# Kernel tuning notes

Hardware: AMD Instinct MI355X
Metric: run time of the kernel (lower is better)

The kernel has to match this reference:

```python
import jax, jax.numpy as jnp
import numpy as np

B, S, D, H, F = 8, 1024, 1024, 16, 4096
DH = D // H
EPS = 1e-8
NEG_INF = -1e30


def setup_inputs() -> dict:
    key = jax.random.key(0)
    ks = jax.random.split(key, 12)
    x = jax.random.normal(ks[0], (B, S, D), jnp.float32)
    # variable valid lengths in [S//2, S]; True = keep (valid token)
    lengths = jax.random.randint(ks[1], (B,), S // 2, S + 1)
    src_key_padding_mask = jnp.arange(S)[None, :] < lengths[:, None]
    rel_pos_bias = 0.02 * jax.random.normal(ks[2], (1, H, S, S), jnp.float32)
    w = lambda k, sh, std: std * jax.random.normal(k, sh, jnp.float32)
    std = D ** -0.5
    return {
        'x': x,
        'src_key_padding_mask': src_key_padding_mask,
        'rel_pos_bias': rel_pos_bias,
        'Wq': w(ks[3], (D, D), std),
        'Wk': w(ks[4], (D, D), std),
        'Wv': w(ks[5], (D, D), std),
        'Wo': w(ks[6], (D, D), std),
        'g1': jnp.ones((D,), jnp.float32),
        'g2': jnp.ones((D,), jnp.float32),
        'W1': w(ks[7], (D, F), std),
        'b1': jnp.zeros((F,), jnp.float32),
        'W2': w(ks[8], (F, F and D), F ** -0.5),
        'b2': jnp.zeros((D,), jnp.float32),
    }


def rmsnorm(x, g):
    # x / sqrt(mean(x^2) + eps) * g   (no mean subtraction)
    ms = jnp.mean(x * x, axis=-1, keepdims=True)
    return x * jax.lax.rsqrt(ms + EPS) * g


def attention(h, kpm, rel_pos_bias, Wq, Wk, Wv, Wo):
    b, s, d = h.shape
    q = (h @ Wq).reshape(b, s, H, DH)
    k = (h @ Wk).reshape(b, s, H, DH)
    v = (h @ Wv).reshape(b, s, H, DH)
    scores = jnp.einsum('bqhd,bkhd->bhqk', q, k) / np.sqrt(DH)
    scores = scores + rel_pos_bias
    scores = jnp.where(kpm[:, None, None, :], scores, NEG_INF)
    attn = jax.nn.softmax(scores, axis=-1)
    out = jnp.einsum('bhqk,bkhd->bqhd', attn, v).reshape(b, s, d)
    return out @ Wo


def reference(x, src_key_padding_mask, rel_pos_bias,
              Wq, Wk, Wv, Wo, g1, g2, W1, b1, W2, b2):
    h = rmsnorm(x, g1)
    x = x + attention(h, src_key_padding_mask, rel_pos_bias, Wq, Wk, Wv, Wo)
    h = rmsnorm(x, g2)
    ff = jax.nn.relu(h @ W1 + b1) @ W2 + b2
    return x + ff
```

## Files before the change

### kernel.cpp

```cpp
#include <hip/hip_runtime.h>
#include <stdint.h>

typedef __bf16 bf16;
typedef __bf16 bf16x4 __attribute__((ext_vector_type(4)));
typedef __bf16 bf16x8 __attribute__((ext_vector_type(8)));
typedef float f32x4 __attribute__((ext_vector_type(4)));

constexpr int Bz = 8, S = 1024, D = 1024, NH = 16, DH = 64, F = 4096;

__device__ __forceinline__ bool is_f32(const uint16_t* dt) { return dt[0] == 0; }

__device__ __forceinline__ void ld4(const void* p, size_t idx, bool f32, float o[4]) {
  if (f32) {
    float4 v = *(const float4*)((const float*)p + idx);
    o[0] = v.x; o[1] = v.y; o[2] = v.z; o[3] = v.w;
  } else {
    bf16x4 v = *(const bf16x4*)((const bf16*)p + idx);
    o[0] = v[0]; o[1] = v[1]; o[2] = v[2]; o[3] = v[3];
  }
}

__device__ __forceinline__ float ld1(const void* p, size_t idx, bool f32) {
  return f32 ? ((const float*)p)[idx] : (float)((const bf16*)p)[idx];
}

__device__ __forceinline__ void gload_lds16(const bf16* g, bf16* l) {
  __builtin_amdgcn_global_load_lds(
      (const __attribute__((address_space(1))) void*)g,
      (__attribute__((address_space(3))) void*)l, 16, 0, 0);
}

__global__ void prep_all(const void* __restrict__ sq, const void* __restrict__ sk,
                         const void* __restrict__ sv, const void* __restrict__ so,
                         const void* __restrict__ s1, const void* __restrict__ s2,
                         bf16* __restrict__ dq, bf16* __restrict__ dk,
                         bf16* __restrict__ dv, bf16* __restrict__ do_,
                         bf16* __restrict__ d1, bf16* __restrict__ d2,
                         const unsigned char* __restrict__ mask,
                         int* __restrict__ lengths,
                         const void* __restrict__ rpb, bf16* __restrict__ biasb,
                         const uint16_t* __restrict__ dt) {
  __shared__ bf16 tile[64][65];
  __shared__ int sred[4];
  bool f32 = is_f32(dt);
  int t = blockIdx.x;
  int tx = threadIdx.x, ty = threadIdx.y;
  if (t >= 3080) {
    size_t i = ((size_t)(t - 3080) * 256 + ty * 16 + tx) * 4;
    float v[4];
    ld4(rpb, i, f32, v);
    bf16x4 o;
#pragma unroll
    for (int j = 0; j < 4; j++) o[j] = (bf16)(v[j] * 1.4426950408889634f);
    *(bf16x4*)(biasb + i) = o;
    return;
  }
  if (t >= 3072) {
    int b = t - 3072;
    int tid = ty * 16 + tx;
    int esz = (mask[1] == 1) ? 1 : ((mask[1] != 0) ? 2 : 4);
    int cnt = 0;
    for (int s = tid; s < S; s += 256) {
      const unsigned char* p = mask + ((size_t)b * S + s) * esz;
      unsigned v = 0;
      for (int j = 0; j < esz; j++) v |= p[j];
      cnt += (v != 0) ? 1 : 0;
    }
#pragma unroll
    for (int m = 32; m >= 1; m >>= 1) cnt += __shfl_xor(cnt, m);
    if ((tid & 63) == 0) sred[tid >> 6] = cnt;
    __syncthreads();
    if (tid == 0) lengths[b] = sred[0] + sred[1] + sred[2] + sred[3];
    return;
  }
  const void* src;
  bf16* dst;
  int R, C, gx, base;
  if (t < 1024) {
    int wsel = t >> 8;
    base = wsel << 8;
    src = wsel == 0 ? sq : wsel == 1 ? sk : wsel == 2 ? sv : so;
    dst = wsel == 0 ? dq : wsel == 1 ? dk : wsel == 2 ? dv : do_;
    R = 1024; C = 1024; gx = 16;
  } else if (t < 2048) {
    base = 1024; src = s1; dst = d1; R = 1024; C = 4096; gx = 64;
  } else {
    base = 2048; src = s2; dst = d2; R = 4096; C = 1024; gx = 16;
  }
  int rel = t - base;
  int c0 = (rel % gx) * 64, r0 = (rel / gx) * 64;
#pragma unroll
  for (int i = 0; i < 4; i++) {
    int r = ty * 4 + i;
    float v[4];
    ld4(src, (size_t)(r0 + r) * C + c0 + tx * 4, f32, v);
#pragma unroll
    for (int j = 0; j < 4; j++) tile[r][tx * 4 + j] = (bf16)v[j];
  }
  __syncthreads();
#pragma unroll
  for (int i = 0; i < 4; i++) {
    int rr = ty * 4 + i;
    bf16x4 ov;
#pragma unroll
    for (int j = 0; j < 4; j++) ov[j] = tile[tx * 4 + j][rr];
    *(bf16x4*)(dst + (size_t)(c0 + rr) * R + r0 + tx * 4) = ov;
  }
}

template <bool ADD>
__global__ void rmsnorm_kernel(const void* __restrict__ xv, const bf16* __restrict__ add,
                               const void* __restrict__ gv, bf16* __restrict__ y,
                               const uint16_t* __restrict__ dt) {
  bool f32 = is_f32(dt);
  int row = blockIdx.x, t = threadIdx.x;
  float xf[4];
  ld4(xv, (size_t)row * D + t * 4, f32, xf);
  if (ADD) {
    bf16x4 a = *(const bf16x4*)(add + (size_t)row * D + t * 4);
#pragma unroll
    for (int j = 0; j < 4; j++) xf[j] += (float)a[j];
  }
  float ss = xf[0] * xf[0] + xf[1] * xf[1] + xf[2] * xf[2] + xf[3] * xf[3];
#pragma unroll
  for (int m = 32; m >= 1; m >>= 1) ss += __shfl_xor(ss, m);
  __shared__ float sred[4];
  if ((t & 63) == 0) sred[t >> 6] = ss;
  __syncthreads();
  float tot = sred[0] + sred[1] + sred[2] + sred[3];
  float scale = rsqrtf(tot * (1.0f / D) + 1e-8f);
  float gf[4];
  ld4(gv, (size_t)t * 4, f32, gf);
  bf16x4 ov;
#pragma unroll
  for (int j = 0; j < 4; j++) ov[j] = (bf16)(xf[j] * scale * gf[j]);
  *(bf16x4*)(y + (size_t)row * D + t * 4) = ov;
}

template <bool BIAS, bool RELU, bool RES1, bool RES2, bool OUTEXT, bool VT>
__global__ void gemm_nt(const bf16* __restrict__ A, const bf16* __restrict__ Bt,
                        void* __restrict__ Cv, const void* __restrict__ biasv,
                        const void* __restrict__ res1, const bf16* __restrict__ res2,
                        int M, int N, int K, const uint16_t* __restrict__ dt) {
  bool f32 = is_f32(dt);
  __shared__ bf16 As[2 * 4096];
  __shared__ bf16 Bs[2 * 4096];
  const int tid = threadIdx.x, lane = tid & 63, w = tid >> 6;
  const int wm = w >> 1, wn = w & 1;
  const int lid = blockIdx.x;
  const int bm = ((lid & 7) << 3) + ((lid >> 3) & 7);
  const int bn = lid >> 6;
  const int quad = lane >> 4, c = lane & 15;

  f32x4 acc[4][4];
#pragma unroll
  for (int i = 0; i < 4; i++)
#pragma unroll
    for (int j = 0; j < 4; j++)
#pragma unroll
      for (int r = 0; r < 4; r++) acc[i][j][r] = 0.f;

  const bf16* gA = A + (size_t)(bm * 128 + w * 16 + (lane >> 2)) * K + (lane & 3) * 8;
  const bf16* gB = Bt + (size_t)(bn * 128 + w * 16 + (lane >> 2)) * K + (lane & 3) * 8;
  bf16* lA = As + w * 512;
  bf16* lB = Bs + w * 512;
  const size_t rstep = (size_t)64 * K;

  int aoff[4], boff[4];
#pragma unroll
  for (int i = 0; i < 4; i++) {
    aoff[i] = (wm * 64 + i * 16 + c) * 32 + quad * 8;
    boff[i] = (wn * 64 + i * 16 + c) * 32 + quad * 8;
  }

  for (int k0 = 0; k0 < K; k0 += 64) {
    __syncthreads();
#pragma unroll
    for (int p = 0; p < 2; p++) {
      gload_lds16(gA + p * 32, lA + p * 4096);
      gload_lds16(gA + p * 32 + rstep, lA + p * 4096 + 2048);
      gload_lds16(gB + p * 32, lB + p * 4096);
      gload_lds16(gB + p * 32 + rstep, lB + p * 4096 + 2048);
    }
    gA += 64;
    gB += 64;
    __syncthreads();
#pragma unroll
    for (int p = 0; p < 2; p++) {
      bf16x8 af[4], bfr[4];
#pragma unroll
      for (int i = 0; i < 4; i++) af[i] = *(const bf16x8*)(As + p * 4096 + aoff[i]);
#pragma unroll
      for (int i = 0; i < 4; i++) bfr[i] = *(const bf16x8*)(Bs + p * 4096 + boff[i]);
#pragma unroll
      for (int i = 0; i < 4; i++)
#pragma unroll
        for (int j = 0; j < 4; j++)
          acc[i][j] = __builtin_amdgcn_mfma_f32_16x16x32_bf16(af[i], bfr[j], acc[i][j], 0, 0, 0);
    }
  }

  const int m0 = bm * 128 + wm * 64, n0 = bn * 128 + wn * 64;
#pragma unroll
  for (int i = 0; i < 4; i++) {
#pragma unroll
    for (int j = 0; j < 4; j++) {
      int col = n0 + j * 16 + c;
      if (VT) {
        int row0 = m0 + i * 16 + quad * 4;
        int bb = row0 >> 10, s0 = row0 & 1023;
        int hh = col >> 6, dd = col & 63;
        bf16x4 ov;
#pragma unroll
        for (int r = 0; r < 4; r++) ov[r] = (bf16)acc[i][j][r];
        *(bf16x4*)((bf16*)Cv + ((size_t)((bb << 4) + hh) * 64 + dd) * 1024 + s0) = ov;
      } else {
        float bv = BIAS ? ld1(biasv, col, f32) : 0.f;
#pragma unroll
        for (int r = 0; r < 4; r++) {
          int row = m0 + i * 16 + quad * 4 + r;
          size_t idx = (size_t)row * N + col;
          float vv = acc[i][j][r] + bv;
          if (RELU) vv = fmaxf(vv, 0.f);
          if (RES1) vv += ld1(res1, idx, f32);
          if (RES2) vv += (float)res2[idx];
          if (OUTEXT && f32) ((float*)Cv)[idx] = vv;
          else ((bf16*)Cv)[idx] = (bf16)vv;
        }
      }
    }
  }
}

#define SYNC()                            \
  do {                                    \
    __builtin_amdgcn_sched_barrier(0);    \
    __builtin_amdgcn_s_barrier();         \
    __builtin_amdgcn_sched_barrier(0);    \
  } while (0)
#define VMW(n)                                              \
  do {                                                      \
    asm volatile("s_waitcnt vmcnt(" #n ")" ::: "memory");   \
    __builtin_amdgcn_sched_barrier(0);                      \
  } while (0)

#define STA_(nb, rowbase, kb)                                                  \
  do {                                                                         \
    gload_lds16(Ag + (size_t)(rowbase) * K + (kb), &Abuf[nb][(rowbase) * 64]); \
    gload_lds16(Ag + (size_t)((rowbase) + 8) * K + (kb),                       \
                &Abuf[nb][((rowbase) + 8) * 64]);                              \
  } while (0)
#define STB_(nb, rowbase, kb)                                                  \
  do {                                                                         \
    gload_lds16(Bg + (size_t)(rowbase) * K + (kb), &Bbuf[nb][(rowbase) * 64]); \
    gload_lds16(Bg + (size_t)((rowbase) + 8) * K + (kb),                       \
                &Bbuf[nb][((rowbase) + 8) * 64]);                              \
  } while (0)
#define RDA_(MQ, fr, bufsel)                                                          \
  do {                                                                                \
    _Pragma("unroll") for (int ii = 0; ii < 4; ii++) {                                \
      int arow = wm * 128 + ((MQ)*4 + ii) * 16 + c;                                   \
      fr[ii][0] = *(const bf16x8*)&Abuf[bufsel][arow * 64 + ((quad ^ sx) * 8)];       \
      fr[ii][1] = *(const bf16x8*)&Abuf[bufsel][arow * 64 + (((4 + quad) ^ sx) * 8)]; \
    }                                                                                 \
  } while (0)
#define RDB_(NQ, fr, bufsel)                                                          \
  do {                                                                                \
    _Pragma("unroll") for (int jj = 0; jj < 2; jj++) {                                \
      int brow = wn * 64 + ((NQ)*2 + jj) * 16 + c;                                    \
      fr[jj][0] = *(const bf16x8*)&Bbuf[bufsel][brow * 64 + ((quad ^ sx) * 8)];       \
      fr[jj][1] = *(const bf16x8*)&Bbuf[bufsel][brow * 64 + (((4 + quad) ^ sx) * 8)]; \
    }                                                                                 \
  } while (0)

template <int MQ, int NQ>
__device__ __forceinline__ void mm_phase(f32x4 (&acc)[8][4], const bf16x8 (&afr)[4][2],
                                         const bf16x8 (&bfr)[2][2]) {
#pragma unroll
  for (int ii = 0; ii < 4; ii++)
#pragma unroll
    for (int jj = 0; jj < 2; jj++) {
      acc[MQ * 4 + ii][NQ * 2 + jj] = __builtin_amdgcn_mfma_f32_16x16x32_bf16(
          afr[ii][0], bfr[jj][0], acc[MQ * 4 + ii][NQ * 2 + jj], 0, 0, 0);
      acc[MQ * 4 + ii][NQ * 2 + jj] = __builtin_amdgcn_mfma_f32_16x16x32_bf16(
          afr[ii][1], bfr[jj][1], acc[MQ * 4 + ii][NQ * 2 + jj], 0, 0, 0);
    }
}

template <bool BIAS, bool RELU, bool QKV>
__global__ void __launch_bounds__(512, 2) gemm256(
    const bf16* __restrict__ A, const bf16* __restrict__ Bt, bf16* __restrict__ C,
    bf16* __restrict__ C2, const void* __restrict__ biasv, int N, int K,
    const uint16_t* __restrict__ dt) {
  bool f32 = is_f32(dt);
  __shared__ bf16 Abuf[2][256 * 64];
  __shared__ bf16 Bbuf[2][256 * 64];
  const int tid = threadIdx.x, lane = tid & 63, w = tid >> 6;
  const int wm = w >> 2, wn = w & 3;
  const int quad = lane >> 4, c = lane & 15;
  const int sx = c & 7;
  const int nbn = N >> 8;
  const int nwg = gridDim.x;
  const int sid = (blockIdx.x & 7) * (nwg >> 3) + (blockIdx.x >> 3);
  const int bm = sid / nbn, bn = sid % nbn;

  const int lrow = lane >> 3;
  const int lslot = ((lane & 7) ^ lrow) * 8;
  const bf16* Ag = A + (size_t)(bm * 256 + lrow) * K + lslot;
  const bf16* Bg = Bt + (size_t)(bn * 256 + lrow) * K + lslot;

  const int ra0 = wm * 128 + wn * 16;
  const int ra1 = ra0 + 64;
  const int rb0 = (wn >> 1) * 128 + (wn & 1) * 64 + wm * 16;
  const int rb1 = rb0 + 32;

  f32x4 acc[8][4];
#pragma unroll
  for (int i = 0; i < 8; i++)
#pragma unroll
    for (int j = 0; j < 4; j++)
#pragma unroll
      for (int r = 0; r < 4; r++) acc[i][j][r] = 0.f;

  const int nt = K >> 6;

  STA_(0, ra0, 0);
  STA_(0, ra1, 0);
  STB_(0, rb0, 0);
  STB_(0, rb1, 0);
  STA_(1, ra0, 64);
  VMW(2);
  SYNC();

  for (int t = 0; t < nt; ++t) {
    const int buf = t & 1, nb = buf ^ 1;
    const int kb1 = (t + 1) << 6, kb2 = (t + 2) << 6;
    const bool st1 = (t + 1 < nt), st2 = (t + 2 < nt);
    bf16x8 afr[4][2], bfr0[2][2], bfr1[2][2];
    RDA_(0, afr, buf);
    RDB_(0, bfr0, buf);
    if (st1) STA_(nb, ra1, kb1);
    SYNC();
    __builtin_amdgcn_s_setprio(1);
    mm_phase<0, 0>(acc, afr, bfr0);
    __builtin_amdgcn_s_setprio(0);
    VMW(2);
    SYNC();
    RDB_(1, bfr1, buf);
    if (st1) STB_(nb, rb0, kb1);
    SYNC();
    __builtin_amdgcn_s_setprio(1);
    mm_phase<0, 1>(acc, afr, bfr1);
    __builtin_amdgcn_s_setprio(0);
    SYNC();
    RDA_(1, afr, buf);
    if (st2) STA_(buf, ra0, kb2);
    SYNC();
    __builtin_amdgcn_s_setprio(1);
    mm_phase<1, 0>(acc, afr, bfr0);
    __builtin_amdgcn_s_setprio(0);
    SYNC();
    if (st1) STB_(nb, rb1, kb1);
    SYNC();
    __builtin_amdgcn_s_setprio(1);
    mm_phase<1, 1>(acc, afr, bfr1);
    __builtin_amdgcn_s_setprio(0);
    VMW(4);
    SYNC();
  }

  const int m0 = bm * 256 + wm * 128, n0 = bn * 256 + wn * 64;
  if (QKV && n0 >= 2048) {
#pragma unroll
    for (int fi = 0; fi < 8; fi++)
#pragma unroll
      for (int fj = 0; fj < 4; fj++) {
        int vcol = n0 + fj * 16 + c - 2048;
        int hh = vcol >> 6, dd = vcol & 63;
        int row0 = m0 + fi * 16 + quad * 4;
        int bb = row0 >> 10, s0 = row0 & 1023;
        bf16x4 ov;
#pragma unroll
        for (int r = 0; r < 4; r++) ov[r] = (bf16)acc[fi][fj][r];
        *(bf16x4*)(C2 + ((size_t)((bb << 4) + hh) * 64 + dd) * 1024 + s0) = ov;
      }
    return;
  }
  const int ldc = QKV ? 2048 : N;
#pragma unroll
  for (int fi = 0; fi < 8; fi++)
#pragma unroll
    for (int fj = 0; fj < 4; fj++) {
      int col = n0 + fj * 16 + c;
      float bv = BIAS ? ld1(biasv, col, f32) : 0.f;
#pragma unroll
      for (int r = 0; r < 4; r++) {
        int row = m0 + fi * 16 + quad * 4 + r;
        float vv = acc[fi][fj][r] + bv;
        if (RELU) vv = fmaxf(vv, 0.f);
        C[(size_t)row * ldc + col] = (bf16)vv;
      }
    }
}

__global__ void __launch_bounds__(256) attn_kernel(
    const bf16* __restrict__ qk, const bf16* __restrict__ vt,
    const bf16* __restrict__ bias, const int* __restrict__ lengths,
    bf16* __restrict__ out) {
  __shared__ bf16 QPs[64 * 72];
  __shared__ bf16 Ks[2][64][72];
  __shared__ bf16 Vs[2][64][72];
  const int tid = threadIdx.x, lane = tid & 63, w = tid >> 6;
  const int id = blockIdx.x;
  const int qt = id >> 7, b = (id >> 4) & 7, h = id & 15;
  const int len = lengths[b];
  const int quad = lane >> 4, c = lane & 15;
  const int r4 = tid >> 2, c4 = tid & 3;

  {
    size_t qrow = (size_t)(b * S + qt * 64 + r4) * 2048 + h * 64 + c4 * 8;
    *(bf16x8*)&QPs[r4 * 72 + c4 * 8] = *(const bf16x8*)&qk[qrow];
    *(bf16x8*)&QPs[r4 * 72 + 32 + c4 * 8] = *(const bf16x8*)&qk[qrow + 32];
  }
  __syncthreads();
  const bf16x8 a0 = *(const bf16x8*)&QPs[(w * 16 + c) * 72 + quad * 8];
  const bf16x8 a1 = *(const bf16x8*)&QPs[(w * 16 + c) * 72 + 32 + quad * 8];

  bf16* Pw = QPs + w * 16 * 72;
  const int xsw = (quad & 2) << 3;
  const int xsr = (c & 8) << 1;

  float l_[4] = {0.f, 0.f, 0.f, 0.f};
  f32x4 o[4];
#pragma unroll
  for (int ni = 0; ni < 4; ni++)
#pragma unroll
    for (int r = 0; r < 4; r++) o[ni][r] = 0.f;

  const bf16* bbp = bias + (size_t)h * S * S + (size_t)(qt * 64 + w * 16 + quad * 4) * S;
  const int nkt = (len + 63) >> 6;

  const size_t KSTEP = (size_t)64 * 2048;
  const bf16* gk = qk + (size_t)(b * S + r4) * 2048 + 1024 + h * 64 + c4 * 8;
  const bf16* gv = vt + ((size_t)((b * 16 + h) * 64 + r4)) * 1024 + c4 * 8;
  bf16x8 kr0 = *(const bf16x8*)gk;
  bf16x8 kr1 = *(const bf16x8*)(gk + 32);
  bf16x8 vr0 = *(const bf16x8*)gv;
  bf16x8 vr1 = *(const bf16x8*)(gv + 32);
  gk += KSTEP;
  gv += 64;
  *(bf16x8*)&Ks[0][r4][c4 * 8] = kr0;
  *(bf16x8*)&Ks[0][r4][32 + c4 * 8] = kr1;
  *(bf16x8*)&Vs[0][r4][c4 * 8] = vr0;
  *(bf16x8*)&Vs[0][r4][32 + c4 * 8] = vr1;
  if (nkt > 1) {
    kr0 = *(const bf16x8*)gk;
    kr1 = *(const bf16x8*)(gk + 32);
    vr0 = *(const bf16x8*)gv;
    vr1 = *(const bf16x8*)(gv + 32);
    gk += KSTEP;
    gv += 64;
  }
  __syncthreads();

  for (int kt = 0; kt < nkt; kt++) {
    const int buf = kt & 1, nb = buf ^ 1;
    if (kt + 1 < nkt) {
      *(bf16x8*)&Ks[nb][r4][c4 * 8] = kr0;
      *(bf16x8*)&Ks[nb][r4][32 + c4 * 8] = kr1;
      *(bf16x8*)&Vs[nb][r4][c4 * 8] = vr0;
      *(bf16x8*)&Vs[nb][r4][32 + c4 * 8] = vr1;
      if (kt + 2 < nkt) {
        kr0 = *(const bf16x8*)gk;
        kr1 = *(const bf16x8*)(gk + 32);
        vr0 = *(const bf16x8*)gv;
        vr1 = *(const bf16x8*)(gv + 32);
        gk += KSTEP;
        gv += 64;
      }
    }

    bf16 br[4][4];
#pragma unroll
    for (int ni = 0; ni < 4; ni++)
#pragma unroll
      for (int r = 0; r < 4; r++) br[ni][r] = bbp[(size_t)r * S + ni * 16 + c];

    f32x4 s[4];
#pragma unroll
    for (int ni = 0; ni < 4; ni++)
#pragma unroll
      for (int r = 0; r < 4; r++) s[ni][r] = 0.f;
    __builtin_amdgcn_s_setprio(1);
#pragma unroll
    for (int ni = 0; ni < 4; ni++) {
      bf16x8 b0 = *(const bf16x8*)&Ks[buf][ni * 16 + c][quad * 8];
      bf16x8 b1 = *(const bf16x8*)&Ks[buf][ni * 16 + c][32 + quad * 8];
      s[ni] = __builtin_amdgcn_mfma_f32_16x16x32_bf16(a0, b0, s[ni], 0, 0, 0);
      s[ni] = __builtin_amdgcn_mfma_f32_16x16x32_bf16(a1, b1, s[ni], 0, 0, 0);
    }
    __builtin_amdgcn_s_setprio(0);

    const bool full = (kt * 64 + 64 <= len);
#pragma unroll
    for (int ni = 0; ni < 4; ni++) {
      int col = kt * 64 + ni * 16 + c;
      bool valid = full || (col < len);
#pragma unroll
      for (int r = 0; r < 4; r++) {
        float p = valid ? exp2f(fmaf(s[ni][r], 0.18033688011112042f, (float)br[ni][r])) : 0.f;
        s[ni][r] = p;
        l_[r] += p;
      }
    }

#pragma unroll
    for (int ni = 0; ni < 4; ni++)
#pragma unroll
      for (int r = 0; r < 4; r++)
        Pw[(quad * 4 + r) * 72 + ((ni * 16 + c) ^ xsw)] = (bf16)s[ni][r];

    bf16x8 p0 = *(const bf16x8*)&Pw[c * 72 + ((quad * 8) ^ xsr)];
    bf16x8 p1 = *(const bf16x8*)&Pw[c * 72 + ((32 + quad * 8) ^ xsr)];
    __builtin_amdgcn_s_setprio(1);
#pragma unroll
    for (int ni = 0; ni < 4; ni++) {
      bf16x8 vb0 = *(const bf16x8*)&Vs[buf][ni * 16 + c][quad * 8];
      bf16x8 vb1 = *(const bf16x8*)&Vs[buf][ni * 16 + c][32 + quad * 8];
      o[ni] = __builtin_amdgcn_mfma_f32_16x16x32_bf16(p0, vb0, o[ni], 0, 0, 0);
      o[ni] = __builtin_amdgcn_mfma_f32_16x16x32_bf16(p1, vb1, o[ni], 0, 0, 0);
    }
    __builtin_amdgcn_s_setprio(0);
    bbp += 64;
    __syncthreads();
  }

  float inv[4];
#pragma unroll
  for (int r = 0; r < 4; r++) {
    float l = l_[r];
    l += __shfl_xor(l, 1);
    l += __shfl_xor(l, 2);
    l += __shfl_xor(l, 4);
    l += __shfl_xor(l, 8);
    inv[r] = 1.f / l;
  }
#pragma unroll
  for (int ni = 0; ni < 4; ni++)
#pragma unroll
    for (int r = 0; r < 4; r++) {
      size_t idx = ((size_t)(b * S + qt * 64 + w * 16 + quad * 4 + r)) * D + h * 64 + ni * 16 + c;
      out[idx] = (bf16)(o[ni][r] * inv[r]);
    }
}

extern "C" void kernel_launch(void* const* d_in, const int* in_sizes, int n_in,
                              void* d_out, int out_size, void* d_ws, size_t ws_size,
                              hipStream_t stream) {
  const void* x = d_in[0];
  const unsigned char* mask = (const unsigned char*)d_in[1];
  const void* rpb = d_in[2];
  const void* Wq = d_in[3];
  const void* Wk = d_in[4];
  const void* Wv = d_in[5];
  const void* Wo = d_in[6];
  const void* g1 = d_in[7];
  const void* g2 = d_in[8];
  const void* W1 = d_in[9];
  const void* b1 = d_in[10];
  const void* W2 = d_in[11];
  const void* b2 = d_in[12];
  const uint16_t* dt = (const uint16_t*)d_in[7];

  char* ws = (char*)d_ws;
  const size_t MB = 1024 * 1024;
  bf16* WqkT = (bf16*)(ws + 0 * MB);
  bf16* WkT = (bf16*)(ws + 2 * MB);
  bf16* WvT = (bf16*)(ws + 4 * MB);
  bf16* WoT = (bf16*)(ws + 6 * MB);
  bf16* W1T = (bf16*)(ws + 8 * MB);
  bf16* W2T = (bf16*)(ws + 16 * MB);
  bf16* hbuf = (bf16*)(ws + 24 * MB);
  bf16* qkbuf = (bf16*)(ws + 40 * MB);
  bf16* d1buf = (bf16*)(ws + 40 * MB);
  bf16* vtbuf = (bf16*)(ws + 72 * MB);
  bf16* biasb = (bf16*)(ws + 88 * MB);
  bf16* a1b = (bf16*)(ws + 56 * MB);
  int* lens = (int*)d_out;

  prep_all<<<dim3(3080 + 16384), dim3(16, 16), 0, stream>>>(
      Wq, Wk, Wv, Wo, W1, W2, WqkT, WkT, WvT, WoT, W1T, W2T, mask, lens, rpb, biasb, dt);

  rmsnorm_kernel<false><<<dim3(8192), dim3(256), 0, stream>>>(x, nullptr, g1, hbuf, dt);
  gemm256<false, false, true><<<dim3(384), dim3(512), 0, stream>>>(
      hbuf, WqkT, qkbuf, vtbuf, nullptr, 3072, 1024, dt);
  attn_kernel<<<dim3(2048), dim3(256), 0, stream>>>(qkbuf, vtbuf, biasb, lens, hbuf);
  gemm_nt<false, false, false, false, false, false><<<dim3(8 * 64), dim3(256), 0, stream>>>(
      hbuf, WoT, d1buf, nullptr, nullptr, nullptr, 8192, 1024, 1024, dt);
  rmsnorm_kernel<true><<<dim3(8192), dim3(256), 0, stream>>>(x, d1buf, g2, hbuf, dt);
  gemm256<true, true, false><<<dim3(512), dim3(512), 0, stream>>>(
      hbuf, W1T, a1b, nullptr, b1, 4096, 1024, dt);
  gemm_nt<true, false, true, true, true, false><<<dim3(8 * 64), dim3(256), 0, stream>>>(
      a1b, W2T, d_out, b2, x, d1buf, 8192, 1024, 4096, dt);

  (void)in_sizes; (void)n_in; (void)out_size; (void)ws_size;
}
```

Measured before the change: 534.3 us.

## Fold first RMSNorm into prep kernel and double GEMM K-step to 128

The first RMSNorm is moved into the prep_all launch as extra blocks, which removes one kernel launch. Separately, gemm_nt now loads a 128-wide K slab per iteration, with LDS buffers doubled to 64 KB total. This halves the number of barrier pairs per K loop. The larger LDS footprint may lower occupancy of the Wo and W2 GEMMs.

```diff
diff --git a/kernel.cpp b/kernel.cpp
--- a/kernel.cpp
+++ b/kernel.cpp
@@ -39,14 +39,37 @@
                          const unsigned char* __restrict__ mask,
                          int* __restrict__ lengths,
                          const void* __restrict__ rpb, bf16* __restrict__ biasb,
+                         const void* __restrict__ x, const void* __restrict__ g1,
+                         bf16* __restrict__ hbuf,
                          const uint16_t* __restrict__ dt) {
   __shared__ bf16 tile[64][65];
   __shared__ int sred[4];
+  __shared__ float sredf[4];
   bool f32 = is_f32(dt);
   int t = blockIdx.x;
   int tx = threadIdx.x, ty = threadIdx.y;
+  int tid = ty * 16 + tx;
+  if (t >= 19464) {
+    int row = t - 19464;
+    float xf[4];
+    ld4(x, (size_t)row * D + tid * 4, f32, xf);
+    float ss = xf[0] * xf[0] + xf[1] * xf[1] + xf[2] * xf[2] + xf[3] * xf[3];
+#pragma unroll
+    for (int m = 32; m >= 1; m >>= 1) ss += __shfl_xor(ss, m);
+    if ((tid & 63) == 0) sredf[tid >> 6] = ss;
+    __syncthreads();
+    float tot = sredf[0] + sredf[1] + sredf[2] + sredf[3];
+    float scale = rsqrtf(tot * (1.0f / D) + 1e-8f);
+    float gf[4];
+    ld4(g1, (size_t)tid * 4, f32, gf);
+    bf16x4 ov;
+#pragma unroll
+    for (int j = 0; j < 4; j++) ov[j] = (bf16)(xf[j] * scale * gf[j]);
+    *(bf16x4*)(hbuf + (size_t)row * D + tid * 4) = ov;
+    return;
+  }
   if (t >= 3080) {
-    size_t i = ((size_t)(t - 3080) * 256 + ty * 16 + tx) * 4;
+    size_t i = ((size_t)(t - 3080) * 256 + tid) * 4;
     float v[4];
     ld4(rpb, i, f32, v);
     bf16x4 o;
@@ -57,7 +80,6 @@
   }
   if (t >= 3072) {
     int b = t - 3072;
-    int tid = ty * 16 + tx;
     int esz = (mask[1] == 1) ? 1 : ((mask[1] != 0) ? 2 : 4);
     int cnt = 0;
     for (int s = tid; s < S; s += 256) {
@@ -143,8 +165,8 @@
                         const void* __restrict__ res1, const bf16* __restrict__ res2,
                         int M, int N, int K, const uint16_t* __restrict__ dt) {
   bool f32 = is_f32(dt);
-  __shared__ bf16 As[2 * 4096];
-  __shared__ bf16 Bs[2 * 4096];
+  __shared__ bf16 As[4 * 4096];
+  __shared__ bf16 Bs[4 * 4096];
   const int tid = threadIdx.x, lane = tid & 63, w = tid >> 6;
   const int wm = w >> 1, wn = w & 1;
   const int lid = blockIdx.x;
@@ -173,20 +195,20 @@
     boff[i] = (wn * 64 + i * 16 + c) * 32 + quad * 8;
   }
 
-  for (int k0 = 0; k0 < K; k0 += 64) {
+  for (int k0 = 0; k0 < K; k0 += 128) {
     __syncthreads();
 #pragma unroll
-    for (int p = 0; p < 2; p++) {
+    for (int p = 0; p < 4; p++) {
       gload_lds16(gA + p * 32, lA + p * 4096);
       gload_lds16(gA + p * 32 + rstep, lA + p * 4096 + 2048);
       gload_lds16(gB + p * 32, lB + p * 4096);
       gload_lds16(gB + p * 32 + rstep, lB + p * 4096 + 2048);
     }
-    gA += 64;
-    gB += 64;
+    gA += 128;
+    gB += 128;
     __syncthreads();
 #pragma unroll
-    for (int p = 0; p < 2; p++) {
+    for (int p = 0; p < 4; p++) {
       bf16x8 af[4], bfr[4];
 #pragma unroll
       for (int i = 0; i < 4; i++) af[i] = *(const bf16x8*)(As + p * 4096 + aoff[i]);
@@ -588,10 +610,10 @@
   bf16* a1b = (bf16*)(ws + 56 * MB);
   int* lens = (int*)d_out;
 
-  prep_all<<<dim3(3080 + 16384), dim3(16, 16), 0, stream>>>(
-      Wq, Wk, Wv, Wo, W1, W2, WqkT, WkT, WvT, WoT, W1T, W2T, mask, lens, rpb, biasb, dt);
-
-  rmsnorm_kernel<false><<<dim3(8192), dim3(256), 0, stream>>>(x, nullptr, g1, hbuf, dt);
+  prep_all<<<dim3(3080 + 16384 + 8192), dim3(16, 16), 0, stream>>>(
+      Wq, Wk, Wv, Wo, W1, W2, WqkT, WkT, WvT, WoT, W1T, W2T, mask, lens, rpb, biasb,
+      x, g1, hbuf, dt);
+
   gemm256<false, false, true><<<dim3(384), dim3(512), 0, stream>>>(
       hbuf, WqkT, qkbuf, vtbuf, nullptr, 3072, 1024, dt);
   attn_kernel<<<dim3(2048), dim3(256), 0, stream>>>(qkbuf, vtbuf, biasb, lens, hbuf);
```

New measurement: 524.7 us. No clear change (-1.8%).
